# Performance work log

Hardware: AMD Instinct MI355X
Metric: run time of the kernel (lower is better)

Reference implementation:

```python
import jax, jax.numpy as jnp
import numpy as np

HEADS = 8
DIM_HEAD = 64
SCALE = DIM_HEAD ** -0.5
POS_DIM = 64


def _sincos_pe(H, W, dim, dtype):
    # matches build_2d_sincos_pos_embed: [1, dim, H, W]
    y = jnp.linspace(-1.0, 1.0, H)[:, None] * jnp.ones((1, W), jnp.float32)
    x = jnp.ones((H, 1), jnp.float32) * jnp.linspace(-1.0, 1.0, W)[None, :]
    omega = 1.0 / (10000.0 ** (jnp.arange(dim // 4, dtype=jnp.float32) / (dim // 4)))
    px = x[..., None] * omega  # [H, W, dim//4]
    py = y[..., None] * omega
    pe = jnp.concatenate([jnp.sin(px), jnp.cos(px), jnp.sin(py), jnp.cos(py)], axis=-1)
    return pe.transpose(2, 0, 1)[None].astype(dtype)


def _conv2d(x, w):
    return jax.lax.conv_general_dilated(
        x, w, (1, 1), 'SAME', dimension_numbers=('NCHW', 'OIHW', 'NCHW'))


def _sobel(d):
    kx = jnp.array([[1, 0, -1], [2, 0, -2], [1, 0, -1]], jnp.float32).reshape(1, 1, 3, 3)
    ky = jnp.array([[1, 2, 1], [0, 0, 0], [-1, -2, -1]], jnp.float32).reshape(1, 1, 3, 3)
    return _conv2d(d, kx), _conv2d(d, ky)


def setup_inputs() -> dict:
    key = jax.random.key(0)
    ks = jax.random.split(key, 8)
    B, C, H, W = 2, 256, 64, 64
    hid = HEADS * DIM_HEAD  # 512
    s = 0.02
    return {
        'x': jax.random.normal(ks[0], (B, C, H, W), jnp.float32),
        'dsm': jax.random.uniform(ks[1], (B, 1, H, W), jnp.float32),
        'wq': jax.random.normal(ks[2], (hid, C), jnp.float32) * s,
        'wkv': jax.random.normal(ks[3], (2 * hid, C + 1), jnp.float32) * s,
        'wout': jax.random.normal(ks[4], (C, hid), jnp.float32) * s,
        'bout': jnp.zeros((C,), jnp.float32),
        'w_hape': jax.random.normal(ks[5], (hid, POS_DIM + 3), jnp.float32) * s,
        'b_hape': jnp.zeros((hid,), jnp.float32),
        'w_alpha': jax.random.normal(ks[6], (1, 1, 3, 3), jnp.float32) * 0.1,
        'b_alpha': jnp.zeros((1,), jnp.float32),
    }


def reference(x, dsm, wq, wkv, wout, bout, w_hape, b_hape, w_alpha, b_alpha):
    B, C, H, W = x.shape
    hid = wq.shape[0]
    # per-sample min-max normalize DSM over spatial dims
    dmin = dsm.min(axis=(2, 3), keepdims=True)
    dmax = dsm.max(axis=(2, 3), keepdims=True)
    d = (dsm - dmin) / (dmax - dmin + 1e-6)
    # HAPE: [PE | h | grad_h] -> 1x1 conv to hidden
    pe = jnp.broadcast_to(_sincos_pe(H, W, POS_DIM, x.dtype), (B, POS_DIM, H, W))
    gx, gy = _sobel(d)
    hape_in = jnp.concatenate([pe, d, gx, gy], axis=1)  # [B, 67, H, W]
    hape_k = jnp.einsum('oc,bchw->bohw', w_hape, hape_in) + b_hape[None, :, None, None]
    # QKV via 1x1 convs
    q = jnp.einsum('oc,bchw->bohw', wq, x)
    kv = jnp.einsum('oc,bchw->bohw', wkv, jnp.concatenate([x, d], axis=1))
    k = kv[:, :hid] + hape_k
    v = kv[:, hid:]
    to_heads = lambda t: t.reshape(B, HEADS, DIM_HEAD, H * W)  # b (h c) x y -> b h c (xy)
    qh = to_heads(q) * SCALE
    kh = to_heads(k)
    vh = to_heads(v)
    sim = jnp.einsum('bhdi,bhdj->bhij', qh, kh)  # [B, h, N, N]
    attn = jax.nn.softmax(sim, axis=-1)
    out = jnp.einsum('bhij,bhdj->bhid', attn, vh)  # [B, h, N, d]
    # b h (x y) d -> b (h d) x y
    out = out.transpose(0, 1, 3, 2).reshape(B, HEADS * DIM_HEAD, H, W)
    out = jnp.einsum('oc,bchw->bohw', wout, out) + bout[None, :, None, None]
    # fine: gradient-magnitude alpha gating
    mag = jnp.sqrt(jnp.maximum(gx, 0.0) ** 2 + jnp.maximum(gy, 0.0) ** 2 + 1e-12)
    alpha = jax.nn.sigmoid(_conv2d(mag, w_alpha) + b_alpha[None, :, None, None])
    return x + out * alpha
```

## Files before the change

kernel.cpp:

```cpp
#include <hip/hip_runtime.h>
#include <math.h>

#define NPOS 4096
#define MTOT 8192
#define KP   352
#define HT 64
#define WT 64

typedef unsigned short ushortT;
typedef short v8s __attribute__((ext_vector_type(8)));
typedef float v4f __attribute__((ext_vector_type(4)));

static __device__ __forceinline__ ushortT bfr(float f) {
    union { float f; unsigned u; } v; v.f = f;
    return (ushortT)((v.u + 0x8000u) >> 16);
}
static __device__ __forceinline__ unsigned pack2bf(float a, float b) {
    union { float f; unsigned u; } ua, ub; ua.f = a; ub.f = b;
    return __builtin_amdgcn_perm(ub.u + 0x8000u, ua.u + 0x8000u, 0x07060302u);
}
static __device__ __forceinline__ unsigned pack2bf_t(float a, float b) {
    union { float f; unsigned u; } ua, ub; ua.f = a; ub.f = b;
    return __builtin_amdgcn_perm(ub.u, ua.u, 0x07060302u);
}
static __device__ __forceinline__ float bf2f_lo(unsigned v) {
    union { unsigned u; float f; } x; x.u = v << 16; return x.f;
}
static __device__ __forceinline__ float bf2f_hi(unsigned v) {
    union { unsigned u; float f; } x; x.u = v & 0xffff0000u; return x.f;
}
static __device__ __forceinline__ float fexp2(float x) {
#if __has_builtin(__builtin_amdgcn_exp2f)
    return __builtin_amdgcn_exp2f(x);
#else
    return exp2f(x);
#endif
}
static __device__ __forceinline__ void ld_lds16(const ushortT* g, ushortT* l) {
    __builtin_amdgcn_global_load_lds(
        (const __attribute__((address_space(1))) unsigned int*)(const void*)g,
        (__attribute__((address_space(3))) unsigned int*)(void*)l, 16, 0, 0);
}

__global__ void k_minmax(const float* __restrict__ dsm, float* __restrict__ mm) {
    int b = blockIdx.x;
    const float* p = dsm + (size_t)b * NPOS;
    float mn = 1e30f, mx = -1e30f;
    for (int i = threadIdx.x; i < NPOS; i += 256) {
        float v = p[i];
        mn = fminf(mn, v); mx = fmaxf(mx, v);
    }
    for (int off = 32; off; off >>= 1) {
        mn = fminf(mn, __shfl_xor(mn, off, 64));
        mx = fmaxf(mx, __shfl_xor(mx, off, 64));
    }
    __shared__ float smn[4], smx[4];
    int wid = threadIdx.x >> 6;
    if ((threadIdx.x & 63) == 0) { smn[wid] = mn; smx[wid] = mx; }
    __syncthreads();
    if (threadIdx.x == 0) {
        mn = fminf(fminf(smn[0], smn[1]), fminf(smn[2], smn[3]));
        mx = fmaxf(fmaxf(smx[0], smx[1]), fmaxf(smx[2], smx[3]));
        mm[b * 2 + 0] = mn; mm[b * 2 + 1] = mx;
    }
}

__global__ void k_prep(const float* __restrict__ dsm, const float* __restrict__ mm,
                       const float* __restrict__ walpha, const float* __restrict__ balpha,
                       ushortT* __restrict__ F, float* __restrict__ alpha) {
    int idx = blockIdx.x * 256 + threadIdx.x;
    int b = idx / NPOS, n = idx % NPOS;
    int hh = n / WT, ww = n % WT;
    float dmin = mm[b * 2], dmax = mm[b * 2 + 1];
    float inv = 1.0f / (dmax - dmin + 1e-6f);
    const float* dp = dsm + (size_t)b * NPOS;

    float dwin[5][5];
    #pragma unroll
    for (int dy = 0; dy < 5; dy++)
        #pragma unroll
        for (int dx = 0; dx < 5; dx++) {
            int y = hh + dy - 2, x = ww + dx - 2;
            float v = 0.0f;
            if (y >= 0 && y < HT && x >= 0 && x < WT) v = (dp[y * WT + x] - dmin) * inv;
            dwin[dy][dx] = v;
        }

    float gxc = 0.f, gyc = 0.f;
    float conv = 0.f;
    #pragma unroll
    for (int oy = 0; oy < 3; oy++)
        #pragma unroll
        for (int ox = 0; ox < 3; ox++) {
            int qy = hh + oy - 1, qx = ww + ox - 1;
            float m = 0.0f;
            if (qy >= 0 && qy < HT && qx >= 0 && qx < WT) {
                float gx = dwin[oy][ox] - dwin[oy][ox + 2]
                         + 2.f * dwin[oy + 1][ox] - 2.f * dwin[oy + 1][ox + 2]
                         + dwin[oy + 2][ox] - dwin[oy + 2][ox + 2];
                float gy = dwin[oy][ox] + 2.f * dwin[oy][ox + 1] + dwin[oy][ox + 2]
                         - dwin[oy + 2][ox] - 2.f * dwin[oy + 2][ox + 1] - dwin[oy + 2][ox + 2];
                if (oy == 1 && ox == 1) { gxc = gx; gyc = gy; }
                float rx = fmaxf(gx, 0.f), ry = fmaxf(gy, 0.f);
                m = sqrtf(rx * rx + ry * ry + 1e-12f);
            }
            conv += walpha[oy * 3 + ox] * m;
        }
    alpha[idx] = 1.f / (1.f + __expf(-(conv + balpha[0])));

    ushortT* fb = F + (size_t)idx * KP;
    fb[256] = bfr(dwin[2][2]);
    fb[257] = bfr(gxc);
    fb[258] = bfr(gyc);
    float xc = -1.f + 2.f * (float)ww / 63.f;
    float yc = -1.f + 2.f * (float)hh / 63.f;
    const float l2w = 13.287712379549449f;
    #pragma unroll
    for (int i = 0; i < 16; i++) {
        float omega = exp2f(-(float)i * (l2w / 16.f));
        float px = xc * omega, py = yc * omega;
        fb[259 + i]      = bfr(__sinf(px));
        fb[259 + 16 + i] = bfr(__cosf(px));
        fb[259 + 32 + i] = bfr(__sinf(py));
        fb[259 + 48 + i] = bfr(__cosf(py));
    }
    #pragma unroll
    for (int z = 323; z < KP; z++) fb[z] = 0;
}

__global__ void k_cast(const float* __restrict__ x, ushortT* __restrict__ F) {
    __shared__ __align__(16) ushortT Tl[64][72];
    int nt = blockIdx.x * 64;
    int b = blockIdx.y >> 2, ct = (blockIdx.y & 3) * 64;
    int t = threadIdx.x;
    #pragma unroll
    for (int rep = 0; rep < 4; rep++) {
        int row = rep * 16 + (t >> 4), c4 = (t & 15) * 4;
        float4 f4 = *(const float4*)&x[((size_t)(b * 256 + ct + row)) * NPOS + nt + c4];
        Tl[c4 + 0][row] = bfr(f4.x);
        Tl[c4 + 1][row] = bfr(f4.y);
        Tl[c4 + 2][row] = bfr(f4.z);
        Tl[c4 + 3][row] = bfr(f4.w);
    }
    __syncthreads();
    #pragma unroll
    for (int rep = 0; rep < 2; rep++) {
        int slot = rep * 256 + t, row = slot >> 3, c8 = slot & 7;
        *(uint4*)&F[((size_t)(b * 4096 + nt + row)) * KP + ct + c8 * 8] = *(uint4*)&Tl[row][c8 * 8];
    }
}

__global__ void k_wc(const float* __restrict__ wq, const float* __restrict__ wkv,
                     const float* __restrict__ whape, const float* __restrict__ bhape,
                     const float* __restrict__ wout,
                     ushortT* __restrict__ Wc, float* __restrict__ biasc,
                     ushortT* __restrict__ woutb) {
    int bid = blockIdx.x;
    if (bid >= 2112) {
        int idx = (bid - 2112) * 256 + threadIdx.x;
        woutb[idx] = bfr(wout[idx]);
        return;
    }
    int idx = bid * 256 + threadIdx.x;
    int o = idx / KP, k = idx % KP;
    float v = 0.f;
    if (o < 512) {
        if (k < 256) v = wq[o * 256 + k] * 0.18033688011112042f;
        if (k == 0) biasc[o] = 0.f;
    } else if (o < 1024) {
        int r = o - 512;
        if (k < 257) v = wkv[r * 257 + k];
        if (k == 256)      v += whape[r * 67 + 64];
        else if (k == 257) v = whape[r * 67 + 65];
        else if (k == 258) v = whape[r * 67 + 66];
        else if (k >= 259 && k < 323) v = whape[r * 67 + (k - 259)];
        if (k == 0) biasc[o] = bhape[r];
    } else {
        int r = o - 512;
        if (k < 257) v = wkv[r * 257 + k];
        if (k == 0) biasc[o] = 0.f;
    }
    Wc[idx] = bfr(v);
}

__global__ __launch_bounds__(256) void k_gemm1(const ushortT* __restrict__ Wc, const ushortT* __restrict__ F,
                                               const float* __restrict__ biasc,
                                               ushortT* __restrict__ qT, ushortT* __restrict__ kT,
                                               ushortT* __restrict__ vv) {
    __shared__ __align__(16) ushortT Al[64][40];
    __shared__ __align__(16) ushortT Bl[64][40];
    __shared__ __align__(16) ushortT Vt[64][72];
    int mt = blockIdx.x * 64;
    int ot = blockIdx.y * 64;
    int t = threadIdx.x, w = t >> 6, lane = t & 63, u = lane & 15, quad = lane >> 4;
    int arow = t >> 2, ac8 = t & 3;
    v4f acc[4] = {};
    for (int k0 = 0; k0 < KP; k0 += 32) {
        __syncthreads();
        *(uint4*)&Al[arow][ac8 * 8] = *(const uint4*)&Wc[(size_t)(ot + arow) * KP + k0 + ac8 * 8];
        *(uint4*)&Bl[arow][ac8 * 8] = *(const uint4*)&F[(size_t)(mt + arow) * KP + k0 + ac8 * 8];
        __syncthreads();
        v8s a = *(v8s*)&Al[w * 16 + u][quad * 8];
        #pragma unroll
        for (int n4 = 0; n4 < 4; n4++) {
            v8s bb = *(v8s*)&Bl[n4 * 16 + u][quad * 8];
            acc[n4] = __builtin_amdgcn_mfma_f32_16x16x32_bf16(a, bb, acc[n4], 0, 0, 0);
        }
    }
    int obase = ot + w * 16 + quad * 4;
    float bo[4];
    #pragma unroll
    for (int r = 0; r < 4; r++) bo[r] = biasc[obase + r];
    if (ot < 1024) {
        int h = (ot >> 6) & 7;
        ushortT* dst = (ot < 512) ? qT : kT;
        #pragma unroll
        for (int n4 = 0; n4 < 4; n4++) {
            int m = mt + n4 * 16 + u;
            uint2 val;
            val.x = pack2bf(acc[n4][0] + bo[0], acc[n4][1] + bo[1]);
            val.y = pack2bf(acc[n4][2] + bo[2], acc[n4][3] + bo[3]);
            *(uint2*)&dst[((size_t)h * MTOT + m) * 64 + w * 16 + quad * 4] = val;
        }
    } else {
        __syncthreads();
        #pragma unroll
        for (int n4 = 0; n4 < 4; n4++) {
            int ml = n4 * 16 + u;
            #pragma unroll
            for (int r = 0; r < 4; r++) Vt[w * 16 + quad * 4 + r][ml] = bfr(acc[n4][r] + bo[r]);
        }
        __syncthreads();
        #pragma unroll
        for (int rep = 0; rep < 2; rep++) {
            int slot = rep * 256 + t, row = slot >> 3, c8 = slot & 7;
            *(uint4*)&vv[(size_t)(ot - 1024 + row) * MTOT + mt + c8 * 8] = *(uint4*)&Vt[row][c8 * 8];
        }
    }
}

#define FRAG(f) ((f) * 512)
__global__ __launch_bounds__(256, 2) void k_flash(const ushortT* __restrict__ qT,
                                                  const ushortT* __restrict__ kT,
                                                  const ushortT* __restrict__ vv,
                                                  ushortT* __restrict__ OpB,
                                                  float* __restrict__ liPart) {
    __shared__ __align__(16) ushortT Kbuf[2][8 * 512];
    __shared__ __align__(16) ushortT Vbuf[2][8 * 512];
    __shared__ __align__(16) ushortT Pw[4][8 * 512];

    int it = blockIdx.x;
    int bh = blockIdx.y;
    int half = blockIdx.z;
    int b = bh >> 3, h = bh & 7;
    int colbase = b * NPOS;
    int t = threadIdx.x, w = t >> 6, lane = t & 63, u = lane & 15, quad = lane >> 4;
    int qb = it * 256 + w * 64;

    const ushortT* Qg = qT + ((size_t)h * MTOT + colbase + qb) * 64;
    const ushortT* Kg = kT + ((size_t)h * MTOT + colbase + half * 2048) * 64;
    const ushortT* Vg = vv + ((size_t)(h * 64)) * MTOT + colbase + half * 2048;
    ushortT* P = &Pw[w][0];

    v8s bq[4][2];
    #pragma unroll
    for (int g = 0; g < 4; g++)
        #pragma unroll
        for (int hf = 0; hf < 2; hf++)
            bq[g][hf] = *(const v8s*)&Qg[(size_t)(g * 16 + u) * 64 + hf * 32 + quad * 8];

    float li[4] = {0.f, 0.f, 0.f, 0.f};
    v4f O[4][4] = {};

    auto stage = [&](int jb, int bufi) {
        ld_lds16(&Kg[(size_t)(jb + w * 16 + u) * 64 + 0 * 32 + quad * 8], &Kbuf[bufi][FRAG(2 * w + 0)]);
        ld_lds16(&Kg[(size_t)(jb + w * 16 + u) * 64 + 1 * 32 + quad * 8], &Kbuf[bufi][FRAG(2 * w + 1)]);
        ld_lds16(&Vg[(size_t)(w * 16 + u) * MTOT + jb + 0 * 32 + quad * 8], &Vbuf[bufi][FRAG(2 * w + 0)]);
        ld_lds16(&Vg[(size_t)(w * 16 + u) * MTOT + jb + 1 * 32 + quad * 8], &Vbuf[bufi][FRAG(2 * w + 1)]);
    };

    stage(0, 0);
    __syncthreads();

    for (int jc = 0; jc < 32; jc++) {
        int cur = jc & 1;
        if (jc + 1 < 32) stage((jc + 1) * 64, cur ^ 1);
        const ushortT* Kb = &Kbuf[cur][0];
        const ushortT* Vb = &Vbuf[cur][0];

        #pragma unroll
        for (int k4 = 0; k4 < 4; k4++) {
            v8s ak0 = *(const v8s*)&Kb[FRAG(k4 * 2 + 0) + lane * 8];
            v8s ak1 = *(const v8s*)&Kb[FRAG(k4 * 2 + 1) + lane * 8];
            v4f st[4];
            #pragma unroll
            for (int g = 0; g < 4; g++) {
                st[g] = (v4f){0.f, 0.f, 0.f, 0.f};
                st[g] = __builtin_amdgcn_mfma_f32_16x16x32_bf16(ak0, bq[g][0], st[g], 0, 0, 0);
                st[g] = __builtin_amdgcn_mfma_f32_16x16x32_bf16(ak1, bq[g][1], st[g], 0, 0, 0);
            }
            #pragma unroll
            for (int g = 0; g < 4; g++) {
                float p0 = fexp2(st[g][0]);
                float p1 = fexp2(st[g][1]);
                float p2 = fexp2(st[g][2]);
                float p3 = fexp2(st[g][3]);
                li[g] += (p0 + p1) + (p2 + p3);
                uint2 pv; pv.x = pack2bf_t(p0, p1); pv.y = pack2bf_t(p2, p3);
                *(uint2*)&P[FRAG(g * 2 + (k4 >> 1)) +
                            ((((k4 & 1) * 2 + (quad >> 1)) * 16 + u) * 8) + (quad & 1) * 4] = pv;
            }
        }

        v8s bp[4][2];
        #pragma unroll
        for (int g = 0; g < 4; g++)
            #pragma unroll
            for (int ks = 0; ks < 2; ks++)
                bp[g][ks] = *(v8s*)&P[FRAG(g * 2 + ks) + lane * 8];
        #pragma unroll
        for (int d4 = 0; d4 < 4; d4++) {
            v8s av0 = *(const v8s*)&Vb[FRAG(d4 * 2 + 0) + lane * 8];
            v8s av1 = *(const v8s*)&Vb[FRAG(d4 * 2 + 1) + lane * 8];
            #pragma unroll
            for (int g = 0; g < 4; g++) {
                O[d4][g] = __builtin_amdgcn_mfma_f32_16x16x32_bf16(av0, bp[g][0], O[d4][g], 0, 0, 0);
                O[d4][g] = __builtin_amdgcn_mfma_f32_16x16x32_bf16(av1, bp[g][1], O[d4][g], 0, 0, 0);
            }
        }
        __syncthreads();
    }

    #pragma unroll
    for (int g = 0; g < 4; g++) {
        li[g] += __shfl_xor(li[g], 16, 64);
        li[g] += __shfl_xor(li[g], 32, 64);
        size_t m2 = (size_t)(half * 2 + b) * 4096 + qb + g * 16 + u;
        size_t base = m2 * 512 + h * 64;
        #pragma unroll
        for (int d4 = 0; d4 < 4; d4++) {
            uint2 val;
            val.x = pack2bf(O[d4][g][0], O[d4][g][1]);
            val.y = pack2bf(O[d4][g][2], O[d4][g][3]);
            *(uint2*)&OpB[base + d4 * 16 + quad * 4] = val;
        }
        if (quad == 0) liPart[m2 * 8 + h] = li[g];
    }
}

__global__ __launch_bounds__(256) void k_gemm2(const ushortT* __restrict__ woutb, const ushortT* __restrict__ OpB,
                                               const float* __restrict__ liPart,
                                               const float* __restrict__ bout, const float* __restrict__ x,
                                               const float* __restrict__ alpha, float* __restrict__ out) {
    __shared__ __align__(16) ushortT Al[64][40];
    __shared__ __align__(16) ushortT Bl[64][40];
    int mt = blockIdx.x * 64;
    int ot = blockIdx.y * 64;
    int t = threadIdx.x, w = t >> 6, lane = t & 63, u = lane & 15, quad = lane >> 4;
    int arow = t >> 2, ac8 = t & 3;
    int mg = mt + arow;
    v4f acc[4] = {};
    for (int k0 = 0; k0 < 512; k0 += 32) {
        __syncthreads();
        *(uint4*)&Al[arow][ac8 * 8] = *(const uint4*)&woutb[(size_t)(ot + arow) * 512 + k0 + ac8 * 8];
        {
            int col = k0 + ac8 * 8;
            int hh = col >> 6;
            float l = liPart[(size_t)mg * 8 + hh] + liPart[(size_t)(8192 + mg) * 8 + hh];
            float inv = 1.f / l;
            uint4 o0 = *(const uint4*)&OpB[(size_t)mg * 512 + col];
            uint4 o1 = *(const uint4*)&OpB[(size_t)(8192 + mg) * 512 + col];
            uint4 r;
            r.x = pack2bf((bf2f_lo(o0.x) + bf2f_lo(o1.x)) * inv, (bf2f_hi(o0.x) + bf2f_hi(o1.x)) * inv);
            r.y = pack2bf((bf2f_lo(o0.y) + bf2f_lo(o1.y)) * inv, (bf2f_hi(o0.y) + bf2f_hi(o1.y)) * inv);
            r.z = pack2bf((bf2f_lo(o0.z) + bf2f_lo(o1.z)) * inv, (bf2f_hi(o0.z) + bf2f_hi(o1.z)) * inv);
            r.w = pack2bf((bf2f_lo(o0.w) + bf2f_lo(o1.w)) * inv, (bf2f_hi(o0.w) + bf2f_hi(o1.w)) * inv);
            *(uint4*)&Bl[arow][ac8 * 8] = r;
        }
        __syncthreads();
        v8s a = *(v8s*)&Al[w * 16 + u][quad * 8];
        #pragma unroll
        for (int n4 = 0; n4 < 4; n4++) {
            v8s bb = *(v8s*)&Bl[n4 * 16 + u][quad * 8];
            acc[n4] = __builtin_amdgcn_mfma_f32_16x16x32_bf16(a, bb, acc[n4], 0, 0, 0);
        }
    }
    int b = mt >> 12, n0 = mt & 4095;
    int obase = ot + w * 16 + quad * 4;
    float bo[4];
    #pragma unroll
    for (int r = 0; r < 4; r++) bo[r] = bout[obase + r];
    #pragma unroll
    for (int n4 = 0; n4 < 4; n4++) {
        int n = n0 + n4 * 16 + u;
        float al = alpha[(size_t)b * NPOS + n];
        #pragma unroll
        for (int r = 0; r < 4; r++) {
            size_t xi = ((size_t)(b * 256 + obase + r)) * NPOS + n;
            out[xi] = x[xi] + (acc[n4][r] + bo[r]) * al;
        }
    }
}

extern "C" void kernel_launch(void* const* d_in, const int* in_sizes, int n_in,
                              void* d_out, int out_size, void* d_ws, size_t ws_size,
                              hipStream_t stream) {
    const float* x      = (const float*)d_in[0];
    const float* dsm    = (const float*)d_in[1];
    const float* wq     = (const float*)d_in[2];
    const float* wkv    = (const float*)d_in[3];
    const float* wout   = (const float*)d_in[4];
    const float* bout   = (const float*)d_in[5];
    const float* whape  = (const float*)d_in[6];
    const float* bhape  = (const float*)d_in[7];
    const float* walpha = (const float*)d_in[8];
    const float* balpha = (const float*)d_in[9];
    float* out = (float*)d_out;
    float* ws  = (float*)d_ws;

    size_t off = 0;
    float* mm     = ws + off; off += 256;
    float* alpha  = ws + off; off += (size_t)2 * NPOS;
    float* biasc  = ws + off; off += 2048;
    float* liPart = ws + off; off += (size_t)2 * MTOT * 8;
    ushortT* OpB   = (ushortT*)(ws + off); off += (size_t)2 * MTOT * 512 / 2;
    ushortT* F     = (ushortT*)(ws + off); off += (size_t)MTOT * KP / 2;
    ushortT* Wc    = (ushortT*)(ws + off); off += (size_t)1536 * KP / 2;
    ushortT* woutb = (ushortT*)(ws + off); off += (size_t)256 * 512 / 2;
    ushortT* qT    = (ushortT*)(ws + off); off += (size_t)8 * MTOT * 64 / 2;
    ushortT* kT    = (ushortT*)(ws + off); off += (size_t)8 * MTOT * 64 / 2;
    ushortT* vv    = (ushortT*)(ws + off); off += (size_t)512 * MTOT / 2;
    (void)in_sizes; (void)n_in; (void)out_size; (void)ws_size;

    k_minmax<<<2, 256, 0, stream>>>(dsm, mm);
    k_prep<<<32, 256, 0, stream>>>(dsm, mm, walpha, balpha, F, alpha);
    k_cast<<<dim3(64, 8), 256, 0, stream>>>(x, F);
    k_wc<<<2624, 256, 0, stream>>>(wq, wkv, whape, bhape, wout, Wc, biasc, woutb);
    k_gemm1<<<dim3(128, 24), 256, 0, stream>>>(Wc, F, biasc, qT, kT, vv);
    k_flash<<<dim3(16, 16, 2), 256, 0, stream>>>(qT, kT, vv, OpB, liPart);
    k_gemm2<<<dim3(128, 4), 256, 0, stream>>>(woutb, OpB, liPart, bout, x, alpha, out);
}
```

Baseline: 221.1 us.

## Split flash attention keys into quarters with swizzled LDS and register prefetch

The attention kernel now splits the key range four ways instead of two, doubling the grid, and targets three blocks per CU. K/V staging moves from direct global-to-LDS loads into double-buffered shared memory to register prefetch, with a single XOR-swizzled LDS buffer. The QKV GEMM uses 128-row output tiles so each loaded F tile feeds twice as many MFMAs. The output GEMM must now sum four partial results and normalizers, which adds workspace and reduction traffic.

```diff
diff --git a/kernel.cpp b/kernel.cpp
--- a/kernel.cpp
+++ b/kernel.cpp
@@ -36,10 +36,8 @@
     return exp2f(x);
 #endif
 }
-static __device__ __forceinline__ void ld_lds16(const ushortT* g, ushortT* l) {
-    __builtin_amdgcn_global_load_lds(
-        (const __attribute__((address_space(1))) unsigned int*)(const void*)g,
-        (__attribute__((address_space(3))) unsigned int*)(void*)l, 16, 0, 0);
+static __device__ __forceinline__ void barrier_lgkm() {
+    asm volatile("s_waitcnt lgkmcnt(0)\n\ts_barrier" ::: "memory");
 }
 
 __global__ void k_minmax(const float* __restrict__ dsm, float* __restrict__ mm) {
@@ -187,80 +185,104 @@
                                                const float* __restrict__ biasc,
                                                ushortT* __restrict__ qT, ushortT* __restrict__ kT,
                                                ushortT* __restrict__ vv) {
-    __shared__ __align__(16) ushortT Al[64][40];
+    __shared__ __align__(16) ushortT Al[128][40];
     __shared__ __align__(16) ushortT Bl[64][40];
-    __shared__ __align__(16) ushortT Vt[64][72];
+    __shared__ __align__(16) ushortT Vt[128][72];
     int mt = blockIdx.x * 64;
-    int ot = blockIdx.y * 64;
+    int ot = blockIdx.y * 128;
     int t = threadIdx.x, w = t >> 6, lane = t & 63, u = lane & 15, quad = lane >> 4;
-    int arow = t >> 2, ac8 = t & 3;
-    v4f acc[4] = {};
+    v4f acc[2][4] = {};
     for (int k0 = 0; k0 < KP; k0 += 32) {
         __syncthreads();
-        *(uint4*)&Al[arow][ac8 * 8] = *(const uint4*)&Wc[(size_t)(ot + arow) * KP + k0 + ac8 * 8];
-        *(uint4*)&Bl[arow][ac8 * 8] = *(const uint4*)&F[(size_t)(mt + arow) * KP + k0 + ac8 * 8];
-        __syncthreads();
-        v8s a = *(v8s*)&Al[w * 16 + u][quad * 8];
-        #pragma unroll
-        for (int n4 = 0; n4 < 4; n4++) {
-            v8s bb = *(v8s*)&Bl[n4 * 16 + u][quad * 8];
-            acc[n4] = __builtin_amdgcn_mfma_f32_16x16x32_bf16(a, bb, acc[n4], 0, 0, 0);
-        }
-    }
-    int obase = ot + w * 16 + quad * 4;
-    float bo[4];
-    #pragma unroll
-    for (int r = 0; r < 4; r++) bo[r] = biasc[obase + r];
-    if (ot < 1024) {
-        int h = (ot >> 6) & 7;
-        ushortT* dst = (ot < 512) ? qT : kT;
-        #pragma unroll
-        for (int n4 = 0; n4 < 4; n4++) {
-            int m = mt + n4 * 16 + u;
-            uint2 val;
-            val.x = pack2bf(acc[n4][0] + bo[0], acc[n4][1] + bo[1]);
-            val.y = pack2bf(acc[n4][2] + bo[2], acc[n4][3] + bo[3]);
-            *(uint2*)&dst[((size_t)h * MTOT + m) * 64 + w * 16 + quad * 4] = val;
+        #pragma unroll
+        for (int r2 = 0; r2 < 2; r2++) {
+            int s = t + r2 * 256, arow = s >> 2, ac8 = s & 3;
+            *(uint4*)&Al[arow][ac8 * 8] = *(const uint4*)&Wc[(size_t)(ot + arow) * KP + k0 + ac8 * 8];
+        }
+        {
+            int brow = t >> 2, bc8 = t & 3;
+            *(uint4*)&Bl[brow][bc8 * 8] = *(const uint4*)&F[(size_t)(mt + brow) * KP + k0 + bc8 * 8];
+        }
+        __syncthreads();
+        v8s bb[4];
+        #pragma unroll
+        for (int n4 = 0; n4 < 4; n4++) bb[n4] = *(v8s*)&Bl[n4 * 16 + u][quad * 8];
+        #pragma unroll
+        for (int s = 0; s < 2; s++) {
+            v8s a = *(v8s*)&Al[w * 32 + s * 16 + u][quad * 8];
+            #pragma unroll
+            for (int n4 = 0; n4 < 4; n4++)
+                acc[s][n4] = __builtin_amdgcn_mfma_f32_16x16x32_bf16(a, bb[n4], acc[s][n4], 0, 0, 0);
+        }
+    }
+    if (blockIdx.y < 8) {
+        #pragma unroll
+        for (int s = 0; s < 2; s++) {
+            int oo = ot + w * 32 + s * 16;
+            int h = (oo >> 6) & 7;
+            int dcol = (oo & 63) + quad * 4;
+            ushortT* dst = (oo < 512) ? qT : kT;
+            float bo[4];
+            #pragma unroll
+            for (int r = 0; r < 4; r++) bo[r] = biasc[oo + quad * 4 + r];
+            #pragma unroll
+            for (int n4 = 0; n4 < 4; n4++) {
+                int m = mt + n4 * 16 + u;
+                uint2 val;
+                val.x = pack2bf(acc[s][n4][0] + bo[0], acc[s][n4][1] + bo[1]);
+                val.y = pack2bf(acc[s][n4][2] + bo[2], acc[s][n4][3] + bo[3]);
+                *(uint2*)&dst[((size_t)h * MTOT + m) * 64 + dcol] = val;
+            }
         }
     } else {
         __syncthreads();
         #pragma unroll
-        for (int n4 = 0; n4 < 4; n4++) {
-            int ml = n4 * 16 + u;
-            #pragma unroll
-            for (int r = 0; r < 4; r++) Vt[w * 16 + quad * 4 + r][ml] = bfr(acc[n4][r] + bo[r]);
-        }
-        __syncthreads();
-        #pragma unroll
-        for (int rep = 0; rep < 2; rep++) {
+        for (int s = 0; s < 2; s++) {
+            int orow = w * 32 + s * 16 + quad * 4;
+            float bo[4];
+            #pragma unroll
+            for (int r = 0; r < 4; r++) bo[r] = biasc[ot + orow + r];
+            #pragma unroll
+            for (int n4 = 0; n4 < 4; n4++) {
+                int ml = n4 * 16 + u;
+                #pragma unroll
+                for (int r = 0; r < 4; r++) Vt[orow + r][ml] = bfr(acc[s][n4][r] + bo[r]);
+            }
+        }
+        __syncthreads();
+        #pragma unroll
+        for (int rep = 0; rep < 4; rep++) {
             int slot = rep * 256 + t, row = slot >> 3, c8 = slot & 7;
             *(uint4*)&vv[(size_t)(ot - 1024 + row) * MTOT + mt + c8 * 8] = *(uint4*)&Vt[row][c8 * 8];
         }
     }
 }
 
-#define FRAG(f) ((f) * 512)
-__global__ __launch_bounds__(256, 2) void k_flash(const ushortT* __restrict__ qT,
+#define LIDX(row, cb) (((row) << 6) + ((((cb) ^ ((row) & 7))) << 3))
+__global__ __launch_bounds__(256, 3) void k_flash(const ushortT* __restrict__ qT,
                                                   const ushortT* __restrict__ kT,
                                                   const ushortT* __restrict__ vv,
                                                   ushortT* __restrict__ OpB,
                                                   float* __restrict__ liPart) {
-    __shared__ __align__(16) ushortT Kbuf[2][8 * 512];
-    __shared__ __align__(16) ushortT Vbuf[2][8 * 512];
-    __shared__ __align__(16) ushortT Pw[4][8 * 512];
+    __shared__ __align__(16) ushortT Kbuf[64 * 64];
+    __shared__ __align__(16) ushortT Vbuf[64 * 64];
+    __shared__ __align__(16) ushortT Pw[4][64 * 64];
 
     int it = blockIdx.x;
     int bh = blockIdx.y;
-    int half = blockIdx.z;
+    int quarter = blockIdx.z;
     int b = bh >> 3, h = bh & 7;
     int colbase = b * NPOS;
     int t = threadIdx.x, w = t >> 6, lane = t & 63, u = lane & 15, quad = lane >> 4;
     int qb = it * 256 + w * 64;
 
     const ushortT* Qg = qT + ((size_t)h * MTOT + colbase + qb) * 64;
-    const ushortT* Kg = kT + ((size_t)h * MTOT + colbase + half * 2048) * 64;
-    const ushortT* Vg = vv + ((size_t)(h * 64)) * MTOT + colbase + half * 2048;
+    const ushortT* Kg = kT + ((size_t)h * MTOT + colbase + quarter * 1024) * 64;
+    const ushortT* Vg = vv + ((size_t)(h * 64)) * MTOT + colbase + quarter * 1024;
     ushortT* P = &Pw[w][0];
+
+    int row0 = t >> 3, c80 = t & 7;
+    int row1 = (t >> 3) + 32, c81 = t & 7;
 
     v8s bq[4][2];
     #pragma unroll
@@ -272,26 +294,29 @@
     float li[4] = {0.f, 0.f, 0.f, 0.f};
     v4f O[4][4] = {};
 
-    auto stage = [&](int jb, int bufi) {
-        ld_lds16(&Kg[(size_t)(jb + w * 16 + u) * 64 + 0 * 32 + quad * 8], &Kbuf[bufi][FRAG(2 * w + 0)]);
-        ld_lds16(&Kg[(size_t)(jb + w * 16 + u) * 64 + 1 * 32 + quad * 8], &Kbuf[bufi][FRAG(2 * w + 1)]);
-        ld_lds16(&Vg[(size_t)(w * 16 + u) * MTOT + jb + 0 * 32 + quad * 8], &Vbuf[bufi][FRAG(2 * w + 0)]);
-        ld_lds16(&Vg[(size_t)(w * 16 + u) * MTOT + jb + 1 * 32 + quad * 8], &Vbuf[bufi][FRAG(2 * w + 1)]);
-    };
-
-    stage(0, 0);
-    __syncthreads();
-
-    for (int jc = 0; jc < 32; jc++) {
-        int cur = jc & 1;
-        if (jc + 1 < 32) stage((jc + 1) * 64, cur ^ 1);
-        const ushortT* Kb = &Kbuf[cur][0];
-        const ushortT* Vb = &Vbuf[cur][0];
+    uint4 kr0 = *(const uint4*)&Kg[(size_t)row0 * 64 + c80 * 8];
+    uint4 kr1 = *(const uint4*)&Kg[(size_t)row1 * 64 + c81 * 8];
+    uint4 vr0 = *(const uint4*)&Vg[(size_t)row0 * MTOT + c80 * 8];
+    uint4 vr1 = *(const uint4*)&Vg[(size_t)row1 * MTOT + c81 * 8];
+
+    for (int jc = 0; jc < 16; jc++) {
+        *(uint4*)&Kbuf[LIDX(row0, c80)] = kr0;
+        *(uint4*)&Kbuf[LIDX(row1, c81)] = kr1;
+        *(uint4*)&Vbuf[LIDX(row0, c80)] = vr0;
+        *(uint4*)&Vbuf[LIDX(row1, c81)] = vr1;
+        if (jc + 1 < 16) {
+            int jb = (jc + 1) * 64;
+            kr0 = *(const uint4*)&Kg[(size_t)(jb + row0) * 64 + c80 * 8];
+            kr1 = *(const uint4*)&Kg[(size_t)(jb + row1) * 64 + c81 * 8];
+            vr0 = *(const uint4*)&Vg[(size_t)row0 * MTOT + jb + c80 * 8];
+            vr1 = *(const uint4*)&Vg[(size_t)row1 * MTOT + jb + c81 * 8];
+        }
+        barrier_lgkm();
 
         #pragma unroll
         for (int k4 = 0; k4 < 4; k4++) {
-            v8s ak0 = *(const v8s*)&Kb[FRAG(k4 * 2 + 0) + lane * 8];
-            v8s ak1 = *(const v8s*)&Kb[FRAG(k4 * 2 + 1) + lane * 8];
+            v8s ak0 = *(const v8s*)&Kbuf[LIDX(k4 * 16 + u, quad)];
+            v8s ak1 = *(const v8s*)&Kbuf[LIDX(k4 * 16 + u, 4 + quad)];
             v4f st[4];
             #pragma unroll
             for (int g = 0; g < 4; g++) {
@@ -307,8 +332,7 @@
                 float p3 = fexp2(st[g][3]);
                 li[g] += (p0 + p1) + (p2 + p3);
                 uint2 pv; pv.x = pack2bf_t(p0, p1); pv.y = pack2bf_t(p2, p3);
-                *(uint2*)&P[FRAG(g * 2 + (k4 >> 1)) +
-                            ((((k4 & 1) * 2 + (quad >> 1)) * 16 + u) * 8) + (quad & 1) * 4] = pv;
+                *(uint2*)&P[LIDX(g * 16 + u, k4 * 2 + (quad >> 1)) + (quad & 1) * 4] = pv;
             }
         }
 
@@ -317,25 +341,25 @@
         for (int g = 0; g < 4; g++)
             #pragma unroll
             for (int ks = 0; ks < 2; ks++)
-                bp[g][ks] = *(v8s*)&P[FRAG(g * 2 + ks) + lane * 8];
+                bp[g][ks] = *(v8s*)&P[LIDX(g * 16 + u, ks * 4 + quad)];
         #pragma unroll
         for (int d4 = 0; d4 < 4; d4++) {
-            v8s av0 = *(const v8s*)&Vb[FRAG(d4 * 2 + 0) + lane * 8];
-            v8s av1 = *(const v8s*)&Vb[FRAG(d4 * 2 + 1) + lane * 8];
+            v8s av0 = *(const v8s*)&Vbuf[LIDX(d4 * 16 + u, quad)];
+            v8s av1 = *(const v8s*)&Vbuf[LIDX(d4 * 16 + u, 4 + quad)];
             #pragma unroll
             for (int g = 0; g < 4; g++) {
                 O[d4][g] = __builtin_amdgcn_mfma_f32_16x16x32_bf16(av0, bp[g][0], O[d4][g], 0, 0, 0);
                 O[d4][g] = __builtin_amdgcn_mfma_f32_16x16x32_bf16(av1, bp[g][1], O[d4][g], 0, 0, 0);
             }
         }
-        __syncthreads();
+        barrier_lgkm();
     }
 
     #pragma unroll
     for (int g = 0; g < 4; g++) {
         li[g] += __shfl_xor(li[g], 16, 64);
         li[g] += __shfl_xor(li[g], 32, 64);
-        size_t m2 = (size_t)(half * 2 + b) * 4096 + qb + g * 16 + u;
+        size_t m2 = (size_t)quarter * MTOT + colbase + qb + g * 16 + u;
         size_t base = m2 * 512 + h * 64;
         #pragma unroll
         for (int d4 = 0; d4 < 4; d4++) {
@@ -366,15 +390,22 @@
         {
             int col = k0 + ac8 * 8;
             int hh = col >> 6;
-            float l = liPart[(size_t)mg * 8 + hh] + liPart[(size_t)(8192 + mg) * 8 + hh];
+            float l = 0.f;
+            #pragma unroll
+            for (int qq = 0; qq < 4; qq++) l += liPart[(size_t)(qq * MTOT + mg) * 8 + hh];
             float inv = 1.f / l;
-            uint4 o0 = *(const uint4*)&OpB[(size_t)mg * 512 + col];
-            uint4 o1 = *(const uint4*)&OpB[(size_t)(8192 + mg) * 512 + col];
+            uint4 o[4];
+            #pragma unroll
+            for (int qq = 0; qq < 4; qq++) o[qq] = *(const uint4*)&OpB[(size_t)(qq * MTOT + mg) * 512 + col];
             uint4 r;
-            r.x = pack2bf((bf2f_lo(o0.x) + bf2f_lo(o1.x)) * inv, (bf2f_hi(o0.x) + bf2f_hi(o1.x)) * inv);
-            r.y = pack2bf((bf2f_lo(o0.y) + bf2f_lo(o1.y)) * inv, (bf2f_hi(o0.y) + bf2f_hi(o1.y)) * inv);
-            r.z = pack2bf((bf2f_lo(o0.z) + bf2f_lo(o1.z)) * inv, (bf2f_hi(o0.z) + bf2f_hi(o1.z)) * inv);
-            r.w = pack2bf((bf2f_lo(o0.w) + bf2f_lo(o1.w)) * inv, (bf2f_hi(o0.w) + bf2f_hi(o1.w)) * inv);
+            r.x = pack2bf((bf2f_lo(o[0].x) + bf2f_lo(o[1].x) + bf2f_lo(o[2].x) + bf2f_lo(o[3].x)) * inv,
+                          (bf2f_hi(o[0].x) + bf2f_hi(o[1].x) + bf2f_hi(o[2].x) + bf2f_hi(o[3].x)) * inv);
+            r.y = pack2bf((bf2f_lo(o[0].y) + bf2f_lo(o[1].y) + bf2f_lo(o[2].y) + bf2f_lo(o[3].y)) * inv,
+                          (bf2f_hi(o[0].y) + bf2f_hi(o[1].y) + bf2f_hi(o[2].y) + bf2f_hi(o[3].y)) * inv);
+            r.z = pack2bf((bf2f_lo(o[0].z) + bf2f_lo(o[1].z) + bf2f_lo(o[2].z) + bf2f_lo(o[3].z)) * inv,
+                          (bf2f_hi(o[0].z) + bf2f_hi(o[1].z) + bf2f_hi(o[2].z) + bf2f_hi(o[3].z)) * inv);
+            r.w = pack2bf((bf2f_lo(o[0].w) + bf2f_lo(o[1].w) + bf2f_lo(o[2].w) + bf2f_lo(o[3].w)) * inv,
+                          (bf2f_hi(o[0].w) + bf2f_hi(o[1].w) + bf2f_hi(o[2].w) + bf2f_hi(o[3].w)) * inv);
             *(uint4*)&Bl[arow][ac8 * 8] = r;
         }
         __syncthreads();
@@ -422,8 +453,8 @@
     float* mm     = ws + off; off += 256;
     float* alpha  = ws + off; off += (size_t)2 * NPOS;
     float* biasc  = ws + off; off += 2048;
-    float* liPart = ws + off; off += (size_t)2 * MTOT * 8;
-    ushortT* OpB   = (ushortT*)(ws + off); off += (size_t)2 * MTOT * 512 / 2;
+    float* liPart = ws + off; off += (size_t)4 * MTOT * 8;
+    ushortT* OpB   = (ushortT*)(ws + off); off += (size_t)4 * MTOT * 512 / 2;
     ushortT* F     = (ushortT*)(ws + off); off += (size_t)MTOT * KP / 2;
     ushortT* Wc    = (ushortT*)(ws + off); off += (size_t)1536 * KP / 2;
     ushortT* woutb = (ushortT*)(ws + off); off += (size_t)256 * 512 / 2;
@@ -436,7 +467,7 @@
     k_prep<<<32, 256, 0, stream>>>(dsm, mm, walpha, balpha, F, alpha);
     k_cast<<<dim3(64, 8), 256, 0, stream>>>(x, F);
     k_wc<<<2624, 256, 0, stream>>>(wq, wkv, whape, bhape, wout, Wc, biasc, woutb);
-    k_gemm1<<<dim3(128, 24), 256, 0, stream>>>(Wc, F, biasc, qT, kT, vv);
-    k_flash<<<dim3(16, 16, 2), 256, 0, stream>>>(qT, kT, vv, OpB, liPart);
+    k_gemm1<<<dim3(128, 12), 256, 0, stream>>>(Wc, F, biasc, qT, kT, vv);
+    k_flash<<<dim3(16, 16, 4), 256, 0, stream>>>(qT, kT, vv, OpB, liPart);
     k_gemm2<<<dim3(128, 4), 256, 0, stream>>>(woutb, OpB, liPart, bout, x, alpha, out);
 }
```

Result: slower. 464.1 us (+109.9%).
